# Performance work log

Measured on AMD Instinct MI355X. Metric: run time of the kernel, lower is better.

Reference implementation:

```python
import jax, jax.numpy as jnp
import numpy as np

T, B, F, H, N = 256, 256, 128, 1024, 2


def setup_inputs() -> dict:
    key = jax.random.key(0)
    ks = jax.random.split(key, 12)
    s_in = 1.0 / np.sqrt(H)  # PyTorch LSTM/Linear init scale ~ U(-1/sqrt(H), 1/sqrt(H))
    u = lambda k, shape: jax.random.uniform(k, shape, jnp.float32, -s_in, s_in)
    inp = {
        "x": jax.random.normal(ks[0], (T, B, F), jnp.float32),
        "W_ih0": u(ks[1], (4 * H, F)),
        "W_hh0": u(ks[2], (4 * H, H)),
        "b_ih0": u(ks[3], (4 * H,)),
        "b_hh0": u(ks[4], (4 * H,)),
        "W_ih1": u(ks[5], (4 * H, H)),
        "W_hh1": u(ks[6], (4 * H, H)),
        "b_ih1": u(ks[7], (4 * H,)),
        "b_hh1": u(ks[8], (4 * H,)),
        "W_lin": u(ks[9], (F, H)),
        "b_lin": u(ks[10], (F,)),
        "bs": B,
    }
    return inp


def _lstm_layer(x, W_ih, W_hh, b_ih, b_hh):
    # x: (T, B, in), returns out (T, B, H), (h_T, c_T) each (B, H)
    # Precompute input projections for all timesteps in one big GEMM.
    xW = jnp.einsum('tbf,gf->tbg', x, W_ih) + b_ih + b_hh  # (T, B, 4H)
    h0 = jnp.zeros((x.shape[1], W_hh.shape[1]), x.dtype)

    def step(carry, xw_t):
        h, c = carry
        gates = xw_t + h @ W_hh.T  # (B, 4H); PyTorch gate order i, f, g, o
        i, f, g, o = jnp.split(gates, 4, axis=-1)
        c = jax.nn.sigmoid(f) * c + jax.nn.sigmoid(i) * jnp.tanh(g)
        h = jax.nn.sigmoid(o) * jnp.tanh(c)
        return (h, c), h

    (h_T, c_T), out = jax.lax.scan(step, (h0, h0), xW)
    return out, h_T, c_T


def reference(x, W_ih0, W_hh0, b_ih0, b_hh0, W_ih1, W_hh1, b_ih1, b_hh1, W_lin, b_lin, bs):
    # Stacked 2-layer LSTM with zero initial state (self.h is None on fresh call).
    out0, h0_T, c0_T = _lstm_layer(x, W_ih0, W_hh0, b_ih0, b_hh0)
    out1, h1_T, c1_T = _lstm_layer(out0, W_ih1, W_hh1, b_ih1, b_hh1)
    # Original: y = linear(out[0]) -> first timestep of top layer output.
    y = out1[0] @ W_lin.T + b_lin  # (B, F)
    h_n = jnp.stack([h0_T, h1_T])  # (N, B, H)
    c_n = jnp.stack([c0_T, c1_T])  # (N, B, H)
    return y, h_n, c_n
```

## Files before the change

### kernel.cpp

```cpp
#include <hip/hip_runtime.h>
#include <stdint.h>


typedef __bf16 bf16x8 __attribute__((ext_vector_type(8)));
typedef float  f32x4  __attribute__((ext_vector_type(4)));
typedef unsigned short ushort8v __attribute__((ext_vector_type(8)));
typedef unsigned short ushort4v __attribute__((ext_vector_type(4)));
typedef unsigned short ushort2v __attribute__((ext_vector_type(2)));
typedef __attribute__((address_space(1))) unsigned int as1_u32;
typedef __attribute__((address_space(3))) unsigned int as3_u32;

#define T_STEPS 256
#define BATCH   256
#define HDIM    1024
#define GDIM    4096
#define FDIM    128
#define HXSLOT  (BATCH * HDIM)

static __device__ __forceinline__ float bf2f(unsigned short u) {
  union { unsigned int i; float f; } v; v.i = ((unsigned int)u) << 16; return v.f;
}
static __device__ __forceinline__ unsigned short f2bf(float f) {
  return __builtin_bit_cast(unsigned short, (__bf16)f);
}
static __device__ __forceinline__ float sigm(float x) { return 1.f / (1.f + __expf(-x)); }
static __device__ __forceinline__ float tanh_f(float x) { return 2.f / (1.f + __expf(-2.f * x)) - 1.f; }

static __device__ __forceinline__ void vl1_inv() {
  asm volatile("buffer_inv" ::: "memory");
}

__global__ void conv_bf16(const float* __restrict__ s, unsigned short* __restrict__ d, int n) {
  int i = blockIdx.x * 256 + threadIdx.x;
  if (i < n) d[i] = f2bf(s[i]);
}

__global__ void diag_kernel(float* out, int n, float v) {
  int i = blockIdx.x * 256 + threadIdx.x;
  if (i < n) out[i] = v;
}

__device__ __forceinline__ void post_stamp(unsigned int* st, unsigned int gen, bool fast) {
  if (!fast) __builtin_amdgcn_fence(__ATOMIC_RELEASE, "agent");
  __hip_atomic_store(st, gen, __ATOMIC_RELAXED, __HIP_MEMORY_SCOPE_AGENT);
}

__device__ __forceinline__ void poll_all(unsigned int* stamps, unsigned int target) {
  unsigned int* p = stamps + (threadIdx.x & 31) * 32;
  for (unsigned int it = 0; it < (1u << 15); ++it) {
    unsigned int gv = __hip_atomic_load(p, __ATOMIC_RELAXED, __HIP_MEMORY_SCOPE_AGENT);
    if (__all((int)(gv - target) >= 0)) return;
    if (it > 16) __builtin_amdgcn_s_sleep(1);
  }
}

__device__ __forceinline__ void poll_mine(unsigned int* stamps, int g, int kh, unsigned int target) {
  unsigned int* p = stamps + (kh * 16 + g + 4 * ((int)threadIdx.x & 3)) * 32;
  for (unsigned int it = 0; it < (1u << 15); ++it) {
    unsigned int gv = __hip_atomic_load(p, __ATOMIC_RELAXED, __HIP_MEMORY_SCOPE_AGENT);
    if (__all((int)(gv - target) >= 0)) return;
    if (it > 16) __builtin_amdgcn_s_sleep(1);
  }
}

__device__ __forceinline__ void lds_spin(unsigned int* f, unsigned int need) {
  for (unsigned int it = 0; it < (1u << 15); ++it) {
    unsigned int v = __hip_atomic_load(f, __ATOMIC_ACQUIRE, __HIP_MEMORY_SCOPE_WORKGROUP);
    if ((int)(v - need) >= 0) return;
    if (it > 8) __builtin_amdgcn_s_sleep(1);
  }
}

__device__ __forceinline__ void stage_chunks(const unsigned short* __restrict__ hsrc,
                                             unsigned short* AsPtr, int r0, int g, int kh, int lane) {
  #pragma unroll
  for (int q = 0; q < 4; ++q) {
    int c = kh * 16 + g + 4 * q;
    const char* src = (const char*)(hsrc + (size_t)c * 8192 + r0 * 32);
    char* dst = (char*)AsPtr + c * 2048;
    __builtin_amdgcn_global_load_lds((const as1_u32*)(src + lane * 16), (as3_u32*)dst, 16, 0, 0);
    __builtin_amdgcn_global_load_lds((const as1_u32*)(src + 1024 + lane * 16), (as3_u32*)(dst + 1024), 16, 0, 0);
  }
}

__global__ __launch_bounds__(256) void gemm_bt_xw(
    const unsigned short* __restrict__ A,
    const unsigned short* __restrict__ B,
    unsigned short* __restrict__ xw,
    int K)
{
  const int tid = threadIdx.x, lane = tid & 63, w = tid >> 6;
  const int m0 = blockIdx.x * 128;
  const int n0 = blockIdx.y * 128;
  __shared__ unsigned short As[128 * 64];
  __shared__ unsigned short Bs[128 * 64];
  const int mrow0 = (w & 1) * 64, ncol0 = (w >> 1) * 64;
  const int quad = lane >> 4;

  f32x4 acc[4][4];
  #pragma unroll
  for (int i = 0; i < 4; ++i)
    #pragma unroll
    for (int j = 0; j < 4; ++j) acc[i][j] = f32x4{0.f, 0.f, 0.f, 0.f};

  const int kiter = K >> 6;
  for (int ki = 0; ki < kiter; ++ki) {
    const int k0 = ki * 64;
    __syncthreads();
    #pragma unroll
    for (int i = 0; i < 4; ++i) {
      int obase = (w * 4 + i) * 1024;
      int o = obase + lane * 16;
      int row = o >> 7; int kb = o & 127;
      const char* ga = (const char*)A + ((size_t)(m0 + row) * K + k0) * 2 + kb;
      const char* gb = (const char*)B + ((size_t)(n0 + row) * K + k0) * 2 + kb;
      __builtin_amdgcn_global_load_lds((const as1_u32*)ga, (as3_u32*)((char*)As + obase), 16, 0, 0);
      __builtin_amdgcn_global_load_lds((const as1_u32*)gb, (as3_u32*)((char*)Bs + obase), 16, 0, 0);
    }
    __syncthreads();
    #pragma unroll
    for (int kk = 0; kk < 2; ++kk) {
      bf16x8 af[4], bfr[4];
      #pragma unroll
      for (int mt = 0; mt < 4; ++mt)
        af[mt] = *(const bf16x8*)(As + (mrow0 + mt * 16 + (lane & 15)) * 64 + kk * 32 + quad * 8);
      #pragma unroll
      for (int nt = 0; nt < 4; ++nt)
        bfr[nt] = *(const bf16x8*)(Bs + (ncol0 + nt * 16 + (lane & 15)) * 64 + kk * 32 + quad * 8);
      #pragma unroll
      for (int mt = 0; mt < 4; ++mt)
        #pragma unroll
        for (int nt = 0; nt < 4; ++nt)
          acc[mt][nt] = __builtin_amdgcn_mfma_f32_16x16x32_bf16(af[mt], bfr[nt], acc[mt][nt], 0, 0, 0);
    }
  }
  #pragma unroll
  for (int mt = 0; mt < 4; ++mt) {
    int m = m0 + mrow0 + mt * 16 + quad * 4;
    int tl = m >> 8, b = m & 255;
    #pragma unroll
    for (int nt = 0; nt < 4; ++nt) {
      int col = n0 + ncol0 + nt * 16 + (lane & 15);
      ushort4v v;
      v.x = f2bf(acc[mt][nt][0]); v.y = f2bf(acc[mt][nt][1]);
      v.z = f2bf(acc[mt][nt][2]); v.w = f2bf(acc[mt][nt][3]);
      *(ushort4v*)(xw + ((size_t)tl * GDIM + col) * BATCH + b) = v;
    }
  }
}

__device__ __forceinline__ bool probe_chk(unsigned int* probeBuf, unsigned int* stamps,
                                          unsigned int salt, unsigned int target,
                                          unsigned int* flagLds) {
  const int wg = blockIdx.x, mi = wg & 7, ni = wg >> 3;
  const int tid = threadIdx.x;
  if (tid == 0) probeBuf[wg * 32] = salt ^ (unsigned int)wg;
  __syncthreads();
  if (tid == 0)
    __hip_atomic_store(stamps + ni * 32, target, __ATOMIC_RELAXED, __HIP_MEMORY_SCOPE_AGENT);
  poll_all(stamps, target);
  vl1_inv();
  if (tid == 0) {
    unsigned int bad = 0;
    for (int k = 0; k < 32; ++k) {
      int member = mi + 8 * k;
      unsigned int v = probeBuf[member * 32];
      if (v != (salt ^ (unsigned int)member)) bad = 1;
    }
    *flagLds = bad;
  }
  __syncthreads();
  return (*flagLds == 0);
}

__global__ __launch_bounds__(512, 2) void lstm_layer0_kernel(
    const unsigned short* __restrict__ xbf,
    const float* __restrict__ Wih,
    const float* __restrict__ Whh,
    const float* __restrict__ bih,
    const float* __restrict__ bhh,
    unsigned short* __restrict__ slab,
    unsigned short* __restrict__ hx,
    float* __restrict__ cstate,
    int t0, int ch_len, unsigned int gen_base,
    float* __restrict__ dout_h,
    float* __restrict__ dout_c,
    unsigned int* __restrict__ bar,
    unsigned int* __restrict__ probe)
{
  const int tid = threadIdx.x, lane = tid & 63, wv = tid >> 6;
  const int quad = lane >> 4, l15 = lane & 15;
  const int g = wv & 3, kh = wv >> 2;
  const int wg = blockIdx.x;
  const int mi = wg & 7, ni = wg >> 3;
  const int r0 = mi * 32, hc0 = ni * 32;
  unsigned int* stamps = bar + mi * 1024;

  __shared__ unsigned short As[32 * 1024];
  __shared__ float gbuf[8][32][36];
  __shared__ unsigned int cflag[8];
  __shared__ unsigned int flagLds;

  if (tid < 8) cflag[tid] = 0;

  bf16x8 whh[2][16];
  #pragma unroll
  for (int nt = 0; nt < 2; ++nt) {
    #pragma unroll
    for (int sl = 0; sl < 16; ++sl) {
      int jj = ((g + (sl >> 2)) & 3) + 4 * (sl & 3);
      const float* wrow = Whh + (size_t)(g * HDIM + hc0 + nt * 16 + l15) * HDIM + kh * 512 + jj * 32 + quad * 8;
      f32x4 f0 = *(const f32x4*)(wrow);
      f32x4 f1 = *(const f32x4*)(wrow + 4);
      bf16x8 r;
      r[0] = (__bf16)f0[0]; r[1] = (__bf16)f0[1]; r[2] = (__bf16)f0[2]; r[3] = (__bf16)f0[3];
      r[4] = (__bf16)f1[0]; r[5] = (__bf16)f1[1]; r[6] = (__bf16)f1[2]; r[7] = (__bf16)f1[3];
      whh[nt][sl] = r;
    }
  }
  bf16x8 wih[2][2];
  #pragma unroll
  for (int nt = 0; nt < 2; ++nt) {
    const float* wrow = Wih + (size_t)(g * HDIM + hc0 + nt * 16 + l15) * FDIM + kh * 64 + quad * 8;
    #pragma unroll
    for (int kk = 0; kk < 2; ++kk) {
      f32x4 f0 = *(const f32x4*)(wrow + kk * 32);
      f32x4 f1 = *(const f32x4*)(wrow + kk * 32 + 4);
      bf16x8 r;
      r[0] = (__bf16)f0[0]; r[1] = (__bf16)f0[1]; r[2] = (__bf16)f0[2]; r[3] = (__bf16)f0[3];
      r[4] = (__bf16)f1[0]; r[5] = (__bf16)f1[1]; r[6] = (__bf16)f1[2]; r[7] = (__bf16)f1[3];
      wih[nt][kk] = r;
    }
  }

  const int hcl = tid & 31, rg2 = tid >> 5;
  float bias[4];
  #pragma unroll
  for (int b4 = 0; b4 < 4; ++b4)
    bias[b4] = bih[b4 * HDIM + hc0 + hcl] + bhh[b4 * HDIM + hc0 + hcl];

  float c[2];
  #pragma unroll
  for (int r = 0; r < 2; ++r)
    c[r] = (t0 == 0) ? 0.f : cstate[(size_t)(r0 + rg2 * 2 + r) * HDIM + hc0 + hcl];

  unsigned int salt = 0x9E3779B9u ^ (gen_base * 2654435761u);
  bool fast = probe_chk(probe, stamps, salt, gen_base + 1u, &flagLds);

  const int tend = t0 + ch_len;

  if (t0 > 0) {
    stage_chunks(hx + (size_t)((t0 - 1) & 1) * HXSLOT, As, r0, g, kh, lane);
    asm volatile("s_waitcnt vmcnt(0)" ::: "memory");
    if (lane == 0)
      __hip_atomic_store(&cflag[kh * 4 + g], gen_base + 1u, __ATOMIC_RELEASE, __HIP_MEMORY_SCOPE_WORKGROUP);
  }

  f32x4 acc[2][2];
  #pragma unroll
  for (int mt = 0; mt < 2; ++mt)
    #pragma unroll
    for (int nt = 0; nt < 2; ++nt) acc[mt][nt] = f32x4{0.f, 0.f, 0.f, 0.f};
  #pragma unroll
  for (int j = 0; j < 2; ++j) {
    bf16x8 af[2];
    #pragma unroll
    for (int mt = 0; mt < 2; ++mt)
      af[mt] = *(const bf16x8*)(xbf + (size_t)(t0 * BATCH + r0 + mt * 16 + l15) * FDIM + kh * 64 + j * 32 + quad * 8);
    #pragma unroll
    for (int mt = 0; mt < 2; ++mt)
      #pragma unroll
      for (int nt = 0; nt < 2; ++nt)
        acc[mt][nt] = __builtin_amdgcn_mfma_f32_16x16x32_bf16(af[mt], wih[nt][j], acc[mt][nt], 0, 0, 0);
  }

  #pragma unroll 1
  for (int t = t0; t < tend; ++t) {
    if (t > 0) {
      const unsigned int need = gen_base + 1u + (unsigned int)(t - t0);
      #pragma unroll
      for (int sl = 0; sl < 16; ++sl) {
        const int s = sl >> 2, q = sl & 3;
        int sg = (g + s) & 3;
        if (q == 0 && s > 0) lds_spin(&cflag[kh * 4 + sg], need);
        int cidx = kh * 16 + sg + 4 * q;
        bf16x8 af[2];
        #pragma unroll
        for (int mt = 0; mt < 2; ++mt)
          af[mt] = *(const bf16x8*)((const char*)As + cidx * 2048 + (mt * 16 + l15) * 64 + quad * 16);
        #pragma unroll
        for (int mt = 0; mt < 2; ++mt)
          #pragma unroll
          for (int nt = 0; nt < 2; ++nt)
            acc[mt][nt] = __builtin_amdgcn_mfma_f32_16x16x32_bf16(af[mt], whh[nt][sl], acc[mt][nt], 0, 0, 0);
      }
    }

    #pragma unroll
    for (int mt = 0; mt < 2; ++mt)
      #pragma unroll
      for (int nt = 0; nt < 2; ++nt) {
        int hl = nt * 16 + l15;
        int rq = mt * 16 + quad * 4;
        *(f32x4*)&gbuf[wv][hl][rq] = acc[mt][nt];
      }
    __syncthreads();

    unsigned short* hdst = slab + (size_t)(t - t0 + 1) * (BATCH * HDIM);
    unsigned short* hxd  = hx + (size_t)(t & 1) * HXSLOT;
    #pragma unroll
    for (int r = 0; r < 2; ++r) {
      int row = rg2 * 2 + r;
      float gi = gbuf[0][hcl][row] + gbuf[4][hcl][row] + bias[0];
      float gf = gbuf[1][hcl][row] + gbuf[5][hcl][row] + bias[1];
      float gg = gbuf[2][hcl][row] + gbuf[6][hcl][row] + bias[2];
      float go = gbuf[3][hcl][row] + gbuf[7][hcl][row] + bias[3];
      float iv = sigm(gi), fv = sigm(gf), gv = tanh_f(gg), ov = sigm(go);
      float cn = fv * c[r] + iv * gv;
      c[r] = cn;
      float hv = ov * tanh_f(cn);
      unsigned short hb = f2bf(hv);
      hxd[ni * 8192 + (r0 + row) * 32 + hcl] = hb;
      int gidx = (r0 + row) * HDIM + hc0 + hcl;
      hdst[gidx] = hb;
      if (t == tend - 1) cstate[gidx] = cn;
      if (t == T_STEPS - 1) { dout_h[gidx] = hv; dout_c[gidx] = cn; }
    }
    __syncthreads();

    if (t != tend - 1) {
      const unsigned int tgt = gen_base + 2u + (unsigned int)(t - t0);
      if (tid == 0) post_stamp(stamps + ni * 32, tgt, fast);

      #pragma unroll
      for (int mt = 0; mt < 2; ++mt)
        #pragma unroll
        for (int nt = 0; nt < 2; ++nt) acc[mt][nt] = f32x4{0.f, 0.f, 0.f, 0.f};
      #pragma unroll
      for (int j = 0; j < 2; ++j) {
        bf16x8 af[2];
        #pragma unroll
        for (int mt = 0; mt < 2; ++mt)
          af[mt] = *(const bf16x8*)(xbf + (size_t)((t + 1) * BATCH + r0 + mt * 16 + l15) * FDIM + kh * 64 + j * 32 + quad * 8);
        #pragma unroll
        for (int mt = 0; mt < 2; ++mt)
          #pragma unroll
          for (int nt = 0; nt < 2; ++nt)
            acc[mt][nt] = __builtin_amdgcn_mfma_f32_16x16x32_bf16(af[mt], wih[nt][j], acc[mt][nt], 0, 0, 0);
      }

      poll_mine(stamps, g, kh, tgt);
      if (fast) vl1_inv();
      else __builtin_amdgcn_fence(__ATOMIC_ACQUIRE, "agent");
      stage_chunks(hx + (size_t)(t & 1) * HXSLOT, As, r0, g, kh, lane);
      asm volatile("s_waitcnt vmcnt(0)" ::: "memory");
      if (lane == 0)
        __hip_atomic_store(&cflag[kh * 4 + g], tgt, __ATOMIC_RELEASE, __HIP_MEMORY_SCOPE_WORKGROUP);
    }
  }
}

__global__ __launch_bounds__(512, 2) void lstm_layer1_kernel(
    const unsigned short* __restrict__ xw,
    const float* __restrict__ Whh,
    const float* __restrict__ bih,
    const float* __restrict__ bhh,
    unsigned short* __restrict__ hpp,
    float* __restrict__ cstate,
    int t0, int ch_len, unsigned int gen_base,
    unsigned short* __restrict__ h1t0,
    float* __restrict__ dout_h,
    float* __restrict__ dout_c,
    unsigned int* __restrict__ bar,
    unsigned int* __restrict__ probe)
{
  const int tid = threadIdx.x, lane = tid & 63, wv = tid >> 6;
  const int quad = lane >> 4, l15 = lane & 15;
  const int g = wv & 3, kh = wv >> 2;
  const int wg = blockIdx.x;
  const int mi = wg & 7, ni = wg >> 3;
  const int r0 = mi * 32, hc0 = ni * 32;
  unsigned int* stamps = bar + mi * 1024;

  __shared__ unsigned short As[32 * 1024];
  __shared__ float gbuf[8][32][36];
  __shared__ unsigned int cflag[8];
  __shared__ unsigned int flagLds;

  if (tid < 8) cflag[tid] = 0;

  bf16x8 whh[2][16];
  #pragma unroll
  for (int nt = 0; nt < 2; ++nt) {
    #pragma unroll
    for (int sl = 0; sl < 16; ++sl) {
      int jj = ((g + (sl >> 2)) & 3) + 4 * (sl & 3);
      const float* wrow = Whh + (size_t)(g * HDIM + hc0 + nt * 16 + l15) * HDIM + kh * 512 + jj * 32 + quad * 8;
      f32x4 f0 = *(const f32x4*)(wrow);
      f32x4 f1 = *(const f32x4*)(wrow + 4);
      bf16x8 r;
      r[0] = (__bf16)f0[0]; r[1] = (__bf16)f0[1]; r[2] = (__bf16)f0[2]; r[3] = (__bf16)f0[3];
      r[4] = (__bf16)f1[0]; r[5] = (__bf16)f1[1]; r[6] = (__bf16)f1[2]; r[7] = (__bf16)f1[3];
      whh[nt][sl] = r;
    }
  }

  const int hcl = tid & 31, rg2 = tid >> 5;
  float bias[4];
  #pragma unroll
  for (int b4 = 0; b4 < 4; ++b4)
    bias[b4] = bih[b4 * HDIM + hc0 + hcl] + bhh[b4 * HDIM + hc0 + hcl];

  float c[2];
  #pragma unroll
  for (int r = 0; r < 2; ++r)
    c[r] = (t0 == 0) ? 0.f : cstate[(size_t)(r0 + rg2 * 2 + r) * HDIM + hc0 + hcl];

  unsigned int salt = 0xB5297A4Du ^ (gen_base * 2654435761u);
  bool fast = probe_chk(probe, stamps, salt, gen_base + 1u, &flagLds);

  const int tend = t0 + ch_len;

  if (t0 > 0) {
    stage_chunks(hpp + (size_t)((t0 - 1) & 1) * HXSLOT, As, r0, g, kh, lane);
    asm volatile("s_waitcnt vmcnt(0)" ::: "memory");
    if (lane == 0)
      __hip_atomic_store(&cflag[kh * 4 + g], gen_base + 1u, __ATOMIC_RELEASE, __HIP_MEMORY_SCOPE_WORKGROUP);
  }

  float xwv[4][2];
  #pragma unroll
  for (int g4 = 0; g4 < 4; ++g4) {
    const unsigned short* xp =
        xw + ((size_t)0 * GDIM + g4 * HDIM + hc0 + hcl) * BATCH + r0 + rg2 * 2;
    ushort2v u = *(const ushort2v*)xp;
    xwv[g4][0] = bf2f(u.x); xwv[g4][1] = bf2f(u.y);
  }

  #pragma unroll 1
  for (int t = t0; t < tend; ++t) {
    f32x4 acc[2][2];
    #pragma unroll
    for (int mt = 0; mt < 2; ++mt)
      #pragma unroll
      for (int nt = 0; nt < 2; ++nt) acc[mt][nt] = f32x4{0.f, 0.f, 0.f, 0.f};

    if (t > 0) {
      const unsigned int need = gen_base + 1u + (unsigned int)(t - t0);
      #pragma unroll
      for (int sl = 0; sl < 16; ++sl) {
        const int s = sl >> 2, q = sl & 3;
        int sg = (g + s) & 3;
        if (q == 0 && s > 0) lds_spin(&cflag[kh * 4 + sg], need);
        int cidx = kh * 16 + sg + 4 * q;
        bf16x8 af[2];
        #pragma unroll
        for (int mt = 0; mt < 2; ++mt)
          af[mt] = *(const bf16x8*)((const char*)As + cidx * 2048 + (mt * 16 + l15) * 64 + quad * 16);
        #pragma unroll
        for (int mt = 0; mt < 2; ++mt)
          #pragma unroll
          for (int nt = 0; nt < 2; ++nt)
            acc[mt][nt] = __builtin_amdgcn_mfma_f32_16x16x32_bf16(af[mt], whh[nt][sl], acc[mt][nt], 0, 0, 0);
      }
    }

    #pragma unroll
    for (int mt = 0; mt < 2; ++mt)
      #pragma unroll
      for (int nt = 0; nt < 2; ++nt) {
        int hl = nt * 16 + l15;
        int rq = mt * 16 + quad * 4;
        *(f32x4*)&gbuf[wv][hl][rq] = acc[mt][nt];
      }
    __syncthreads();

    unsigned short* hxd = hpp + (size_t)(t & 1) * HXSLOT;
    #pragma unroll
    for (int r = 0; r < 2; ++r) {
      int row = rg2 * 2 + r;
      float gi = gbuf[0][hcl][row] + gbuf[4][hcl][row] + xwv[0][r] + bias[0];
      float gf = gbuf[1][hcl][row] + gbuf[5][hcl][row] + xwv[1][r] + bias[1];
      float gg = gbuf[2][hcl][row] + gbuf[6][hcl][row] + xwv[2][r] + bias[2];
      float go = gbuf[3][hcl][row] + gbuf[7][hcl][row] + xwv[3][r] + bias[3];
      float iv = sigm(gi), fv = sigm(gf), gv = tanh_f(gg), ov = sigm(go);
      float cn = fv * c[r] + iv * gv;
      c[r] = cn;
      float hv = ov * tanh_f(cn);
      unsigned short hb = f2bf(hv);
      hxd[ni * 8192 + (r0 + row) * 32 + hcl] = hb;
      int gidx = (r0 + row) * HDIM + hc0 + hcl;
      if (h1t0 != nullptr && t == 0) h1t0[gidx] = hb;
      if (t == tend - 1) cstate[gidx] = cn;
      if (t == T_STEPS - 1) { dout_h[gidx] = hv; dout_c[gidx] = cn; }
    }
    __syncthreads();

    if (t != tend - 1) {
      const unsigned int tgt = gen_base + 2u + (unsigned int)(t - t0);
      if (tid == 0) post_stamp(stamps + ni * 32, tgt, fast);

      #pragma unroll
      for (int g4 = 0; g4 < 4; ++g4) {
        const unsigned short* xp =
            xw + ((size_t)(t + 1 - t0) * GDIM + g4 * HDIM + hc0 + hcl) * BATCH + r0 + rg2 * 2;
        ushort2v u = *(const ushort2v*)xp;
        xwv[g4][0] = bf2f(u.x); xwv[g4][1] = bf2f(u.y);
      }

      poll_mine(stamps, g, kh, tgt);
      if (fast) vl1_inv();
      else __builtin_amdgcn_fence(__ATOMIC_ACQUIRE, "agent");
      stage_chunks(hpp + (size_t)(t & 1) * HXSLOT, As, r0, g, kh, lane);
      asm volatile("s_waitcnt vmcnt(0)" ::: "memory");
      if (lane == 0)
        __hip_atomic_store(&cflag[kh * 4 + g], tgt, __ATOMIC_RELEASE, __HIP_MEMORY_SCOPE_WORKGROUP);
    }
  }
}

__global__ void y_kernel(const unsigned short* __restrict__ h1t0,
                         const unsigned short* __restrict__ wlin,
                         const float* __restrict__ blin,
                         float* __restrict__ y)
{
  int b = blockIdx.x;
  int f = threadIdx.x;
  const ushort8v* hp = (const ushort8v*)(h1t0 + (size_t)b * HDIM);
  const ushort8v* wp = (const ushort8v*)(wlin + (size_t)f * HDIM);
  float acc = 0.f;
  for (int i = 0; i < HDIM / 8; ++i) {
    ushort8v hv = hp[i], wvv = wp[i];
    #pragma unroll
    for (int j = 0; j < 8; ++j) acc += bf2f(hv[j]) * bf2f(wvv[j]);
  }
  y[b * FDIM + f] = acc + blin[f];
}

extern "C" void kernel_launch(void* const* d_in, const int* in_sizes, int n_in,
                              void* d_out, int out_size, void* d_ws, size_t ws_size,
                              hipStream_t stream) {
  (void)in_sizes; (void)n_in; (void)out_size;
  const float* x    = (const float*)d_in[0];
  const float* Wih0 = (const float*)d_in[1];
  const float* Whh0 = (const float*)d_in[2];
  const float* bih0 = (const float*)d_in[3];
  const float* bhh0 = (const float*)d_in[4];
  const float* Wih1 = (const float*)d_in[5];
  const float* Whh1 = (const float*)d_in[6];
  const float* bih1 = (const float*)d_in[7];
  const float* bhh1 = (const float*)d_in[8];
  const float* Wlin = (const float*)d_in[9];
  const float* blin = (const float*)d_in[10];
  float* out = (float*)d_out;

  const size_t SZ_BAR   = 32768;
  const size_t SZ_PROBE = 32768;
  const size_t SZ_XBF   = (size_t)T_STEPS * BATCH * FDIM * 2;
  const size_t SZ_WIH1  = (size_t)GDIM * HDIM * 2;
  const size_t SZ_WLIN  = (size_t)FDIM * HDIM * 2;
  const size_t SZ_HPP   = (size_t)2 * BATCH * HDIM * 2;
  const size_t SZ_HX    = (size_t)2 * BATCH * HDIM * 2;
  const size_t SZ_H1T0  = (size_t)BATCH * HDIM * 2;
  const size_t SZ_CST   = (size_t)BATCH * HDIM * 4;
  const size_t SLOT     = (size_t)BATCH * HDIM * 2;
  const size_t fixed = SZ_BAR + SZ_PROBE + SZ_XBF + SZ_WIH1 + SZ_WLIN + SZ_HPP + SZ_HX + SZ_H1T0 + 2 * SZ_CST;

  int CH = 0;
  const int cands[5] = {64, 32, 16, 8, 4};
  for (int i = 0; i < 5; ++i) {
    int c = cands[i];
    size_t need = fixed + (size_t)(c + 1) * SLOT + (size_t)c * GDIM * BATCH * 2;
    if (need <= ws_size) { CH = c; break; }
  }
  if (CH == 0) {
    float v = 1.0e6f + (float)(ws_size >> 20);
    diag_kernel<<<(32768 + 255) / 256, 256, 0, stream>>>(out, 32768, v);
    return;
  }

  char* ws = (char*)d_ws;
  size_t o = 0;
  unsigned int*   bar   = (unsigned int*)(ws + o);    o += SZ_BAR;
  unsigned int*   probe = (unsigned int*)(ws + o);    o += SZ_PROBE;
  unsigned short* xbf   = (unsigned short*)(ws + o);  o += SZ_XBF;
  unsigned short* wih1b = (unsigned short*)(ws + o);  o += SZ_WIH1;
  unsigned short* wlinb = (unsigned short*)(ws + o);  o += SZ_WLIN;
  unsigned short* h1pp  = (unsigned short*)(ws + o);  o += SZ_HPP;
  unsigned short* hx0   = (unsigned short*)(ws + o);  o += SZ_HX;
  unsigned short* h1t0  = (unsigned short*)(ws + o);  o += SZ_H1T0;
  float*          c0st  = (float*)(ws + o);           o += SZ_CST;
  float*          c1st  = (float*)(ws + o);           o += SZ_CST;
  unsigned short* slab  = (unsigned short*)(ws + o);  o += (size_t)(CH + 1) * SLOT;
  unsigned short* xw1   = (unsigned short*)(ws + o);  o += (size_t)CH * GDIM * BATCH * 2;

  hipMemsetAsync(bar, 0, SZ_BAR, stream);

  conv_bf16<<<(T_STEPS * BATCH * FDIM + 255) / 256, 256, 0, stream>>>(x, xbf, T_STEPS * BATCH * FDIM);
  conv_bf16<<<(GDIM * HDIM + 255) / 256, 256, 0, stream>>>(Wih1, wih1b, GDIM * HDIM);
  conv_bf16<<<(FDIM * HDIM + 255) / 256, 256, 0, stream>>>(Wlin, wlinb, FDIM * HDIM);

  float* hn0 = out + 32768;
  float* hn1 = out + 32768 + 262144;
  float* cn0 = out + 32768 + 524288;
  float* cn1 = out + 32768 + 524288 + 262144;

  unsigned int gen_base = 0;
  for (int ch = 0; ch < T_STEPS / CH; ++ch) {
    int t0 = ch * CH;
    lstm_layer0_kernel<<<256, 512, 0, stream>>>(
        xbf, Wih0, Whh0, bih0, bhh0, slab, hx0, c0st, t0, CH, gen_base, hn0, cn0, bar, probe);
    gen_base += (unsigned int)CH;
    gemm_bt_xw<<<dim3(CH * 2, 32), 256, 0, stream>>>(
        slab + BATCH * HDIM, wih1b, xw1, HDIM);
    lstm_layer1_kernel<<<256, 512, 0, stream>>>(
        xw1, Whh1, bih1, bhh1, h1pp, c1st, t0, CH, gen_base, h1t0, hn1, cn1, bar, probe);
    gen_base += (unsigned int)CH;
  }

  y_kernel<<<256, 128, 0, stream>>>(h1t0, wlinb, blin, out);
}
```

Baseline: 3.624 ms.

## Swizzle LDS h-chunk layout, pad gate buffer, tune spin waits and chunk size

Applies an XOR swizzle to the byte offsets of the staged hidden-state chunks. The swizzle is applied both where producers write hx to global and where consumers read A fragments from LDS, with the aim of avoiding LDS bank conflicts. The gate buffer padding changes from 36 to 33 floats and the vector store becomes scalar stores, which also targets bank conflicts. Spin loops now poll longer before sleeping, and larger time-chunk sizes (256, 128) are allowed when workspace permits, reducing the number of chunk launches. Risks: scalar stores add instructions, and the swizzle must match the consumer layout exactly.

```diff
diff --git a/kernel.cpp b/kernel.cpp
--- a/kernel.cpp
+++ b/kernel.cpp
@@ -26,6 +26,10 @@
 static __device__ __forceinline__ float sigm(float x) { return 1.f / (1.f + __expf(-x)); }
 static __device__ __forceinline__ float tanh_f(float x) { return 2.f / (1.f + __expf(-2.f * x)) - 1.f; }
 
+static __device__ __forceinline__ int swz(int b) {
+  return b ^ (((b >> 7) & 3) << 4);
+}
+
 static __device__ __forceinline__ void vl1_inv() {
   asm volatile("buffer_inv" ::: "memory");
 }
@@ -59,7 +63,7 @@
   for (unsigned int it = 0; it < (1u << 15); ++it) {
     unsigned int gv = __hip_atomic_load(p, __ATOMIC_RELAXED, __HIP_MEMORY_SCOPE_AGENT);
     if (__all((int)(gv - target) >= 0)) return;
-    if (it > 16) __builtin_amdgcn_s_sleep(1);
+    if (it > 64) __builtin_amdgcn_s_sleep(1);
   }
 }
 
@@ -67,7 +71,7 @@
   for (unsigned int it = 0; it < (1u << 15); ++it) {
     unsigned int v = __hip_atomic_load(f, __ATOMIC_ACQUIRE, __HIP_MEMORY_SCOPE_WORKGROUP);
     if ((int)(v - need) >= 0) return;
-    if (it > 8) __builtin_amdgcn_s_sleep(1);
+    if (it > 32) __builtin_amdgcn_s_sleep(1);
   }
 }
 
@@ -197,7 +201,7 @@
   unsigned int* stamps = bar + mi * 1024;
 
   __shared__ unsigned short As[32 * 1024];
-  __shared__ float gbuf[8][32][36];
+  __shared__ float gbuf[8][32][33];
   __shared__ unsigned int cflag[8];
   __shared__ unsigned int flagLds;
 
@@ -286,8 +290,11 @@
         int cidx = kh * 16 + sg + 4 * q;
         bf16x8 af[2];
         #pragma unroll
-        for (int mt = 0; mt < 2; ++mt)
-          af[mt] = *(const bf16x8*)((const char*)As + cidx * 2048 + (mt * 16 + l15) * 64 + quad * 16);
+        for (int mt = 0; mt < 2; ++mt) {
+          int bo = (mt * 16 + l15) * 64 + quad * 16;
+          bo = swz(bo);
+          af[mt] = *(const bf16x8*)((const char*)As + cidx * 2048 + bo);
+        }
         #pragma unroll
         for (int mt = 0; mt < 2; ++mt)
           #pragma unroll
@@ -302,7 +309,9 @@
       for (int nt = 0; nt < 2; ++nt) {
         int hl = nt * 16 + l15;
         int rq = mt * 16 + quad * 4;
-        *(f32x4*)&gbuf[wv][hl][rq] = acc[mt][nt];
+        #pragma unroll
+        for (int i = 0; i < 4; ++i)
+          gbuf[wv][hl][rq + i] = acc[mt][nt][i];
       }
     __syncthreads();
 
@@ -320,7 +329,8 @@
       c[r] = cn;
       float hv = ov * tanh_f(cn);
       unsigned short hb = f2bf(hv);
-      hxd[ni * 8192 + (r0 + row) * 32 + hcl] = hb;
+      int boff = swz(row * 64 + hcl * 2);
+      hxd[ni * 8192 + mi * 1024 + (boff >> 1)] = hb;
       int gidx = (r0 + row) * HDIM + hc0 + hcl;
       hdst[gidx] = hb;
       if (t == tend - 1) cstate[gidx] = cn;
@@ -383,7 +393,7 @@
   unsigned int* stamps = bar + mi * 1024;
 
   __shared__ unsigned short As[32 * 1024];
-  __shared__ float gbuf[8][32][36];
+  __shared__ float gbuf[8][32][33];
   __shared__ unsigned int cflag[8];
   __shared__ unsigned int flagLds;
 
@@ -455,8 +465,11 @@
         int cidx = kh * 16 + sg + 4 * q;
         bf16x8 af[2];
         #pragma unroll
-        for (int mt = 0; mt < 2; ++mt)
-          af[mt] = *(const bf16x8*)((const char*)As + cidx * 2048 + (mt * 16 + l15) * 64 + quad * 16);
+        for (int mt = 0; mt < 2; ++mt) {
+          int bo = (mt * 16 + l15) * 64 + quad * 16;
+          bo = swz(bo);
+          af[mt] = *(const bf16x8*)((const char*)As + cidx * 2048 + bo);
+        }
         #pragma unroll
         for (int mt = 0; mt < 2; ++mt)
           #pragma unroll
@@ -471,7 +484,9 @@
       for (int nt = 0; nt < 2; ++nt) {
         int hl = nt * 16 + l15;
         int rq = mt * 16 + quad * 4;
-        *(f32x4*)&gbuf[wv][hl][rq] = acc[mt][nt];
+        #pragma unroll
+        for (int i = 0; i < 4; ++i)
+          gbuf[wv][hl][rq + i] = acc[mt][nt][i];
       }
     __syncthreads();
 
@@ -488,7 +503,8 @@
       c[r] = cn;
       float hv = ov * tanh_f(cn);
       unsigned short hb = f2bf(hv);
-      hxd[ni * 8192 + (r0 + row) * 32 + hcl] = hb;
+      int boff = swz(row * 64 + hcl * 2);
+      hxd[ni * 8192 + mi * 1024 + (boff >> 1)] = hb;
       int gidx = (r0 + row) * HDIM + hc0 + hcl;
       if (h1t0 != nullptr && t == 0) h1t0[gidx] = hb;
       if (t == tend - 1) cstate[gidx] = cn;
@@ -567,8 +583,8 @@
   const size_t fixed = SZ_BAR + SZ_PROBE + SZ_XBF + SZ_WIH1 + SZ_WLIN + SZ_HPP + SZ_HX + SZ_H1T0 + 2 * SZ_CST;
 
   int CH = 0;
-  const int cands[5] = {64, 32, 16, 8, 4};
-  for (int i = 0; i < 5; ++i) {
+  const int cands[7] = {256, 128, 64, 32, 16, 8, 4};
+  for (int i = 0; i < 7; ++i) {
     int c = cands[i];
     size_t need = fixed + (size_t)(c + 1) * SLOT + (size_t)c * GDIM * BATCH * 2;
     if (need <= ws_size) { CH = c; break; }
```

Result: faster. 3.548 ms (-2.1%).
